# Kernel optimization log

Measured on AMD Instinct MI355X. Metric: run time of the kernel, lower is better.

Reference implementation:

```python
import jax, jax.numpy as jnp
import numpy as np

N_SRC = 50000
N_DST = 50000
E = 800000
D = 64


def setup_inputs() -> dict:
    key = jax.random.key(0)
    k1, k2, k3, k4 = jax.random.split(key, 4)
    src_emb = jax.random.normal(k1, (N_SRC, D), dtype=jnp.float32)
    e_att = jax.random.uniform(k2, (E, 1), dtype=jnp.float32)
    src_idx = jax.random.randint(k3, (E,), 0, N_SRC, dtype=jnp.int64)
    dst_idx = jax.random.randint(k4, (E,), 0, N_DST, dtype=jnp.int64)
    return {"src_emb": src_emb, "e_att": e_att, "src_idx": src_idx, "dst_idx": dst_idx}


def reference(src_emb, e_att, src_idx, dst_idx):
    # DGL: fn.src_mul_edge('emb_o','att','msg') then fn.sum('msg','emb_n')
    # msg[e] = src_emb[src_idx[e]] * e_att[e]  -> scatter-sum into dst nodes
    msg = src_emb[src_idx] * e_att                      # [E, D]
    emb_n = jax.ops.segment_sum(msg, dst_idx, num_segments=N_DST)  # [N_DST, D]
    return emb_n
```

## Files before the change

kernel.cpp:

```cpp
#include <hip/hip_runtime.h>
#include <hip/hip_fp16.h>


#define D 64
#define CAP 64
#define OVF_CAP 65536
#define NPART 8

__global__ void __launch_bounds__(256)
convert_emb_kernel(const float* __restrict__ src, __half* __restrict__ dst, int n4,
                   int* __restrict__ cursor, int ncur) {
    int i = blockIdx.x * blockDim.x + threadIdx.x;
    if (i < ncur) cursor[i] = 0;
    if (i >= n4) return;
    float4 v = ((const float4*)src)[i];
    ushort4 h;
    h.x = __half_as_ushort(__float2half(v.x));
    h.y = __half_as_ushort(__float2half(v.y));
    h.z = __half_as_ushort(__float2half(v.z));
    h.w = __half_as_ushort(__float2half(v.w));
    ((ushort4*)dst)[i] = h;
}

__global__ void __launch_bounds__(256)
scatter_xcd_kernel(const int* __restrict__ dst_idx, const int* __restrict__ src_idx,
                   const float* __restrict__ e_att, int* __restrict__ cursor,
                   unsigned* __restrict__ payload,
                   int* __restrict__ ovf_count, int* __restrict__ ovf_list,
                   int E, int n_dst, int rpx, int epb) {
    int x     = blockIdx.x & (NPART - 1);
    int chunk = blockIdx.x >> 3;
    int e0 = chunk * epb;
    int e1 = min(e0 + epb, E);
    int lo = x * rpx;
    int hi = min(lo + rpx, n_dst);

    for (int e = e0 + threadIdx.x; e < e1; e += 256) {
        int d = dst_idx[e];
        if (d < lo || d >= hi) continue;
        int p = atomicAdd(&cursor[d], 1);
        if (p < CAP) {
            unsigned pl = (unsigned)src_idx[e] |
                          ((unsigned)__half_as_ushort(__float2half(e_att[e])) << 16);
            payload[(size_t)d * CAP + p] = pl;
        } else {
            int oi = atomicAdd(ovf_count, 1);
            if (oi < OVF_CAP) ovf_list[oi] = e;
        }
    }
}

__global__ void __launch_bounds__(256)
gather_xcd_kernel(const __half* __restrict__ emb_h,
                  const unsigned* __restrict__ payload,
                  const int* __restrict__ cursor,
                  const int* __restrict__ dst_idx, const int* __restrict__ src_idx,
                  const float* __restrict__ e_att, const float* __restrict__ src_emb,
                  const int* __restrict__ ovf_count, const int* __restrict__ ovf_list,
                  float* __restrict__ out, int n_dst, int rpx) {
    int x    = blockIdx.x & (NPART - 1);
    int g    = blockIdx.x >> 3;
    int wv   = threadIdx.x >> 6;
    int lane = threadIdx.x & 63;
    int local = g * 4 + wv;
    if (local >= rpx) return;
    int w = x * rpx + local;
    if (w >= n_dst) return;

    int cn  = cursor[w];
    int cnt = min(cn, CAP);

    unsigned plv = payload[(size_t)w * CAP + lane];
    int pli = (int)plv;

    float acc = 0.f;
    int j = 0;
    for (; j + 4 <= cnt; j += 4) {
        unsigned p0 = (unsigned)__builtin_amdgcn_readlane(pli, j);
        unsigned p1 = (unsigned)__builtin_amdgcn_readlane(pli, j + 1);
        unsigned p2 = (unsigned)__builtin_amdgcn_readlane(pli, j + 2);
        unsigned p3 = (unsigned)__builtin_amdgcn_readlane(pli, j + 3);
        float a0 = __half2float(__ushort_as_half((unsigned short)(p0 >> 16)));
        float a1 = __half2float(__ushort_as_half((unsigned short)(p1 >> 16)));
        float a2 = __half2float(__ushort_as_half((unsigned short)(p2 >> 16)));
        float a3 = __half2float(__ushort_as_half((unsigned short)(p3 >> 16)));
        float v0 = __half2float(emb_h[(size_t)(p0 & 0xffff) * D + lane]);
        float v1 = __half2float(emb_h[(size_t)(p1 & 0xffff) * D + lane]);
        float v2 = __half2float(emb_h[(size_t)(p2 & 0xffff) * D + lane]);
        float v3 = __half2float(emb_h[(size_t)(p3 & 0xffff) * D + lane]);
        acc = fmaf(v0, a0, acc);
        acc = fmaf(v1, a1, acc);
        acc = fmaf(v2, a2, acc);
        acc = fmaf(v3, a3, acc);
    }
    for (; j < cnt; ++j) {
        unsigned pv = (unsigned)__builtin_amdgcn_readlane(pli, j);
        float a = __half2float(__ushort_as_half((unsigned short)(pv >> 16)));
        acc = fmaf(__half2float(emb_h[(size_t)(pv & 0xffff) * D + lane]), a, acc);
    }

    if (cn > CAP) {
        int oc = *ovf_count;
        if (oc > OVF_CAP) oc = OVF_CAP;
        for (int i = 0; i < oc; ++i) {
            int e = ovf_list[i];
            if (dst_idx[e] == w) {
                float a = e_att[e];
                int   s = src_idx[e];
                acc = fmaf(src_emb[(size_t)s * D + lane], a, acc);
            }
        }
    }

    out[(size_t)w * D + lane] = acc;
}

__global__ void __launch_bounds__(256)
atomic_fallback_kernel(const float* __restrict__ src_emb, const float* __restrict__ e_att,
                       const int* __restrict__ src_idx, const int* __restrict__ dst_idx,
                       float* __restrict__ out, int E) {
    int tid  = blockIdx.x * blockDim.x + threadIdx.x;
    int e    = tid >> 4;
    int part = tid & 15;
    if (e >= E) return;
    int   s = src_idx[e];
    int   d = dst_idx[e];
    float a = e_att[e];
    float4 v = ((const float4*)src_emb)[(size_t)s * 16 + part];
    float* orow = out + (size_t)d * D + part * 4;
    atomicAdd(orow + 0, v.x * a);
    atomicAdd(orow + 1, v.y * a);
    atomicAdd(orow + 2, v.z * a);
    atomicAdd(orow + 3, v.w * a);
}

extern "C" void kernel_launch(void* const* d_in, const int* in_sizes, int n_in,
                              void* d_out, int out_size, void* d_ws, size_t ws_size,
                              hipStream_t stream) {
    const float* src_emb = (const float*)d_in[0];
    const float* e_att   = (const float*)d_in[1];
    const int*   src_idx = (const int*)d_in[2];
    const int*   dst_idx = (const int*)d_in[3];
    float*       out     = (float*)d_out;

    const int E     = in_sizes[2];
    const int n_dst = out_size / D;
    const int n_src = in_sizes[0] / D;

    size_t off_emb = 0;
    size_t off_pay = off_emb + (size_t)n_src * D / 2;
    size_t off_cur = off_pay + (size_t)n_dst * CAP;
    size_t need_ints = off_cur + (size_t)n_dst + 1 + OVF_CAP;

    if (n_src <= 65536 && ws_size >= need_ints * sizeof(int)) {
        __half*   emb_h   = (__half*)d_ws;
        unsigned* payload = (unsigned*)d_ws + off_pay;
        int*      cursor  = (int*)d_ws + off_cur;
        int*      ovf_count = cursor + n_dst;
        int*      ovf_list  = ovf_count + 1;

        const int n4 = n_src * D / 4;
        convert_emb_kernel<<<(n4 + 255) / 256, 256, 0, stream>>>(
            src_emb, emb_h, n4, cursor, n_dst + 1);

        const int rpx = (n_dst + NPART - 1) / NPART;
        const int chunks = 512;
        const int epb    = (E + chunks - 1) / chunks;
        scatter_xcd_kernel<<<chunks * NPART, 256, 0, stream>>>(
            dst_idx, src_idx, e_att, cursor, payload, ovf_count, ovf_list,
            E, n_dst, rpx, epb);

        const int gpb = (rpx + 3) / 4;
        gather_xcd_kernel<<<gpb * NPART, 256, 0, stream>>>(
            emb_h, payload, cursor, dst_idx, src_idx, e_att, src_emb,
            ovf_count, ovf_list, out, n_dst, rpx);
        return;
    }

    hipMemsetAsync(d_out, 0, (size_t)out_size * sizeof(float), stream);
    atomic_fallback_kernel<<<(E * 16 + 255) / 256, 256, 0, stream>>>(
        src_emb, e_att, src_idx, dst_idx, out, E);
}
```

Measured before the change: 134.9 us.

## Vectorize scatter index loads and process two rows per wave in gather

The scatter kernel now reads dst/src/att as int4/float4, so each thread handles four edges per iteration, with a separate tail loop for leftover edges. The gather kernel assigns two destination rows per 64-lane wave, 32 lanes each, and each lane loads a __half2 and accumulates a float2. Payload indices are broadcast with shuffles instead of readlane, and source indices are clamped so padded slots stay in bounds. The aim is fewer load instructions and higher memory-level parallelism. In exchange, both rows in a wave loop to the larger of their two edge counts, and lanes for rows that run out early do masked, wasted work.

```diff
diff --git a/kernel.cpp b/kernel.cpp
--- a/kernel.cpp
+++ b/kernel.cpp
@@ -27,92 +27,124 @@
                    const float* __restrict__ e_att, int* __restrict__ cursor,
                    unsigned* __restrict__ payload,
                    int* __restrict__ ovf_count, int* __restrict__ ovf_list,
-                   int E, int n_dst, int rpx, int epb) {
+                   int E, int n_dst, int rpx, int epb4) {
     int x     = blockIdx.x & (NPART - 1);
     int chunk = blockIdx.x >> 3;
-    int e0 = chunk * epb;
-    int e1 = min(e0 + epb, E);
     int lo = x * rpx;
     int hi = min(lo + rpx, n_dst);
 
-    for (int e = e0 + threadIdx.x; e < e1; e += 256) {
-        int d = dst_idx[e];
-        if (d < lo || d >= hi) continue;
-        int p = atomicAdd(&cursor[d], 1);
-        if (p < CAP) {
-            unsigned pl = (unsigned)src_idx[e] |
-                          ((unsigned)__half_as_ushort(__float2half(e_att[e])) << 16);
-            payload[(size_t)d * CAP + p] = pl;
-        } else {
-            int oi = atomicAdd(ovf_count, 1);
-            if (oi < OVF_CAP) ovf_list[oi] = e;
+    int E4 = E >> 2;
+    int i0 = chunk * epb4;
+    int i1 = min(i0 + epb4, E4);
+
+    for (int i = i0 + threadIdx.x; i < i1; i += 256) {
+        int4   d4 = ((const int4*)dst_idx)[i];
+        int4   s4 = ((const int4*)src_idx)[i];
+        float4 a4 = ((const float4*)e_att)[i];
+        int   dd[4] = {d4.x, d4.y, d4.z, d4.w};
+        int   ss[4] = {s4.x, s4.y, s4.z, s4.w};
+        float aa[4] = {a4.x, a4.y, a4.z, a4.w};
+#pragma unroll
+        for (int k = 0; k < 4; ++k) {
+            int d = dd[k];
+            if (d < lo || d >= hi) continue;
+            int p = atomicAdd(&cursor[d], 1);
+            unsigned pay = (unsigned)ss[k] |
+                           ((unsigned)__half_as_ushort(__float2half(aa[k])) << 16);
+            if (p < CAP) {
+                payload[(size_t)d * CAP + p] = pay;
+            } else {
+                int oi = atomicAdd(ovf_count, 1);
+                if (oi < OVF_CAP) ovf_list[oi] = 4 * i + k;
+            }
         }
     }
-}
-
-__global__ void __launch_bounds__(256)
-gather_xcd_kernel(const __half* __restrict__ emb_h,
-                  const unsigned* __restrict__ payload,
-                  const int* __restrict__ cursor,
-                  const int* __restrict__ dst_idx, const int* __restrict__ src_idx,
-                  const float* __restrict__ e_att, const float* __restrict__ src_emb,
-                  const int* __restrict__ ovf_count, const int* __restrict__ ovf_list,
-                  float* __restrict__ out, int n_dst, int rpx) {
+    if (chunk == 0) {
+        for (int e = (E4 << 2) + threadIdx.x; e < E; e += 256) {
+            int d = dst_idx[e];
+            if (d < lo || d >= hi) continue;
+            int p = atomicAdd(&cursor[d], 1);
+            unsigned pay = (unsigned)src_idx[e] |
+                           ((unsigned)__half_as_ushort(__float2half(e_att[e])) << 16);
+            if (p < CAP) payload[(size_t)d * CAP + p] = pay;
+            else { int oi = atomicAdd(ovf_count, 1); if (oi < OVF_CAP) ovf_list[oi] = e; }
+        }
+    }
+}
+
+__global__ void __launch_bounds__(256)
+gather2_kernel(const __half* __restrict__ emb_h,
+               const unsigned* __restrict__ payload,
+               const int* __restrict__ cursor,
+               const int* __restrict__ dst_idx, const int* __restrict__ src_idx,
+               const float* __restrict__ e_att, const float* __restrict__ src_emb,
+               const int* __restrict__ ovf_count, const int* __restrict__ ovf_list,
+               float* __restrict__ out, int n_dst, int n_src, int rpx) {
     int x    = blockIdx.x & (NPART - 1);
     int g    = blockIdx.x >> 3;
     int wv   = threadIdx.x >> 6;
     int lane = threadIdx.x & 63;
-    int local = g * 4 + wv;
-    if (local >= rpx) return;
+    int sub  = lane >> 5;
+    int l31  = lane & 31;
+
+    int local = (g * 4 + wv) * 2 + sub;
     int w = x * rpx + local;
-    if (w >= n_dst) return;
-
-    int cn  = cursor[w];
+    bool rowvalid = (local < rpx) && (w < n_dst);
+
+    int cn = rowvalid ? cursor[w] : 0;
     int cnt = min(cn, CAP);
 
-    unsigned plv = payload[(size_t)w * CAP + lane];
-    int pli = (int)plv;
-
-    float acc = 0.f;
-    int j = 0;
-    for (; j + 4 <= cnt; j += 4) {
-        unsigned p0 = (unsigned)__builtin_amdgcn_readlane(pli, j);
-        unsigned p1 = (unsigned)__builtin_amdgcn_readlane(pli, j + 1);
-        unsigned p2 = (unsigned)__builtin_amdgcn_readlane(pli, j + 2);
-        unsigned p3 = (unsigned)__builtin_amdgcn_readlane(pli, j + 3);
-        float a0 = __half2float(__ushort_as_half((unsigned short)(p0 >> 16)));
-        float a1 = __half2float(__ushort_as_half((unsigned short)(p1 >> 16)));
-        float a2 = __half2float(__ushort_as_half((unsigned short)(p2 >> 16)));
-        float a3 = __half2float(__ushort_as_half((unsigned short)(p3 >> 16)));
-        float v0 = __half2float(emb_h[(size_t)(p0 & 0xffff) * D + lane]);
-        float v1 = __half2float(emb_h[(size_t)(p1 & 0xffff) * D + lane]);
-        float v2 = __half2float(emb_h[(size_t)(p2 & 0xffff) * D + lane]);
-        float v3 = __half2float(emb_h[(size_t)(p3 & 0xffff) * D + lane]);
-        acc = fmaf(v0, a0, acc);
-        acc = fmaf(v1, a1, acc);
-        acc = fmaf(v2, a2, acc);
-        acc = fmaf(v3, a3, acc);
-    }
-    for (; j < cnt; ++j) {
-        unsigned pv = (unsigned)__builtin_amdgcn_readlane(pli, j);
-        float a = __half2float(__ushort_as_half((unsigned short)(pv >> 16)));
-        acc = fmaf(__half2float(emb_h[(size_t)(pv & 0xffff) * D + lane]), a, acc);
-    }
-
-    if (cn > CAP) {
-        int oc = *ovf_count;
-        if (oc > OVF_CAP) oc = OVF_CAP;
-        for (int i = 0; i < oc; ++i) {
-            int e = ovf_list[i];
-            if (dst_idx[e] == w) {
-                float a = e_att[e];
-                int   s = src_idx[e];
-                acc = fmaf(src_emb[(size_t)s * D + lane], a, acc);
+    uint2 pp = make_uint2(0u, 0u);
+    if (rowvalid) pp = ((const uint2*)(payload + (size_t)w * CAP))[l31];
+
+    int cmax = max(cnt, __shfl_xor(cnt, 32));
+
+    float2 acc = make_float2(0.f, 0.f);
+    unsigned smax = (unsigned)(n_src - 1);
+    for (int j = 0; j < cmax; j += 4) {
+        int sl = (sub << 5) | (j >> 1);
+        unsigned pv0 = (unsigned)__shfl((int)pp.x, sl);
+        unsigned pv1 = (unsigned)__shfl((int)pp.y, sl);
+        unsigned pv2 = (unsigned)__shfl((int)pp.x, sl + 1);
+        unsigned pv3 = (unsigned)__shfl((int)pp.y, sl + 1);
+        float a0 = (j     < cnt) ? __half2float(__ushort_as_half((unsigned short)(pv0 >> 16))) : 0.f;
+        float a1 = (j + 1 < cnt) ? __half2float(__ushort_as_half((unsigned short)(pv1 >> 16))) : 0.f;
+        float a2 = (j + 2 < cnt) ? __half2float(__ushort_as_half((unsigned short)(pv2 >> 16))) : 0.f;
+        float a3 = (j + 3 < cnt) ? __half2float(__ushort_as_half((unsigned short)(pv3 >> 16))) : 0.f;
+        unsigned s0 = min(pv0 & 0xffffu, smax);
+        unsigned s1 = min(pv1 & 0xffffu, smax);
+        unsigned s2 = min(pv2 & 0xffffu, smax);
+        unsigned s3 = min(pv3 & 0xffffu, smax);
+        __half2 h0 = ((const __half2*)(emb_h + (size_t)s0 * D))[l31];
+        __half2 h1 = ((const __half2*)(emb_h + (size_t)s1 * D))[l31];
+        __half2 h2 = ((const __half2*)(emb_h + (size_t)s2 * D))[l31];
+        __half2 h3 = ((const __half2*)(emb_h + (size_t)s3 * D))[l31];
+        acc.x = fmaf(__low2float(h0),  a0, acc.x);
+        acc.y = fmaf(__high2float(h0), a0, acc.y);
+        acc.x = fmaf(__low2float(h1),  a1, acc.x);
+        acc.y = fmaf(__high2float(h1), a1, acc.y);
+        acc.x = fmaf(__low2float(h2),  a2, acc.x);
+        acc.y = fmaf(__high2float(h2), a2, acc.y);
+        acc.x = fmaf(__low2float(h3),  a3, acc.x);
+        acc.y = fmaf(__high2float(h3), a3, acc.y);
+    }
+
+    if (rowvalid) {
+        if (cn > CAP) {
+            int oc = *ovf_count;
+            if (oc > OVF_CAP) oc = OVF_CAP;
+            for (int i = 0; i < oc; ++i) {
+                int e = ovf_list[i];
+                if (dst_idx[e] == w) {
+                    float a = e_att[e];
+                    int   s = src_idx[e];
+                    acc.x = fmaf(src_emb[(size_t)s * D + 2 * l31],     a, acc.x);
+                    acc.y = fmaf(src_emb[(size_t)s * D + 2 * l31 + 1], a, acc.y);
+                }
             }
         }
-    }
-
-    out[(size_t)w * D + lane] = acc;
+        ((float2*)(out + (size_t)w * D))[l31] = acc;
+    }
 }
 
 __global__ void __launch_bounds__(256)
@@ -165,15 +197,16 @@
 
         const int rpx = (n_dst + NPART - 1) / NPART;
         const int chunks = 512;
-        const int epb    = (E + chunks - 1) / chunks;
+        const int E4 = E >> 2;
+        const int epb4 = (E4 + chunks - 1) / chunks;
         scatter_xcd_kernel<<<chunks * NPART, 256, 0, stream>>>(
             dst_idx, src_idx, e_att, cursor, payload, ovf_count, ovf_list,
-            E, n_dst, rpx, epb);
-
-        const int gpb = (rpx + 3) / 4;
-        gather_xcd_kernel<<<gpb * NPART, 256, 0, stream>>>(
+            E, n_dst, rpx, epb4);
+
+        const int gpb = (rpx + 7) / 8;
+        gather2_kernel<<<gpb * NPART, 256, 0, stream>>>(
             emb_h, payload, cursor, dst_idx, src_idx, e_att, src_emb,
-            ovf_count, ovf_list, out, n_dst, rpx);
+            ovf_count, ovf_list, out, n_dst, n_src, rpx);
         return;
     }
 
```

Measured after the change: 131.1 us. 1.03x faster.
